# Optimization experiments

Measured on AMD Instinct MI355X. Metric: run time of the kernel, lower is better.

The kernel has to match this reference:

```python
import jax, jax.numpy as jnp
import numpy as np

N_OBJ = 256   # number of RoIs/objects
C = 151       # num_obj_classes (Visual Genome)
H = 512       # hidden_dim == output_dim
T = 3         # time_step


def setup_inputs() -> dict:
    key = jax.random.key(0)
    ks = jax.random.split(key, 12)
    s = jnp.float32(0.02)

    def lin(k, out_dim, in_dim):
        k1, k2 = jax.random.split(k)
        w = jax.random.normal(k1, (out_dim, in_dim), jnp.float32) * s
        b = jax.random.normal(k2, (out_dim,), jnp.float32) * s
        return w, b

    inp = {}
    inp['input_ggnn'] = jax.random.normal(ks[0], (N_OBJ, H), jnp.float32)
    inp['matrix'] = jax.random.uniform(ks[1], (C, C), jnp.float32)
    for i, name in enumerate(['eq3_w', 'eq3_u', 'eq4_w', 'eq4_u', 'eq5_w', 'eq5_u']):
        in_dim = 2 * H if name.endswith('_w') else H
        w, b = lin(ks[2 + i], H, in_dim)
        inp['w_' + name] = w
        inp['b_' + name] = b
    w, b = lin(ks[8], H, 2 * H)
    inp['w_out'], inp['b_out'] = w, b
    w, b = lin(ks[9], C, C * H)
    inp['w_cls'], inp['b_cls'] = w, b
    return inp


def _ggnn_obj(input_ggnn, matrix,
              w_eq3_w, b_eq3_w, w_eq3_u, b_eq3_u,
              w_eq4_w, b_eq4_w, w_eq4_u, b_eq4_u,
              w_eq5_w, b_eq5_w, w_eq5_u, b_eq5_u,
              w_out, b_out, w_cls, b_cls):
    n = input_ggnn.shape[0]
    # hidden[i, c] = input_ggnn[i] for every class slot c  -> [N, C, H]
    hidden0 = jnp.broadcast_to(input_ggnn[:, None, :], (n, C, H))

    def step(hidden, _):
        hidden_sum = hidden.sum(axis=0)                # [C, H]
        x = hidden_sum[None, :, :] - hidden            # [N, C, H]
        # matrix.T @ x_i  and  matrix @ x_i, vectorized over N
        av1 = jnp.einsum('cd,nch->ndh', matrix, x)     # M^T propagation
        av2 = jnp.einsum('dc,nch->ndh', matrix, x)     # M propagation
        av = jnp.concatenate([av1, av2], axis=-1).reshape(n * C, 2 * H)
        h = hidden.reshape(n * C, H)
        zv = jax.nn.sigmoid(av @ w_eq3_w.T + b_eq3_w + h @ w_eq3_u.T + b_eq3_u)
        rv = jax.nn.sigmoid(av @ w_eq4_w.T + b_eq4_w + h @ w_eq4_u.T + b_eq4_u)
        hv = jnp.tanh(av @ w_eq5_w.T + b_eq5_w + (rv * h) @ w_eq5_u.T + b_eq5_u)
        h = (1.0 - zv) * h + zv * hv
        return h.reshape(n, C, H), None

    hidden, _ = jax.lax.scan(step, hidden0, None, length=T)

    inp_rep = hidden0.reshape(n * C, H)                # input repeated per class slot
    out = jnp.concatenate([hidden.reshape(n * C, H), inp_rep], axis=1)  # [N*C, 2H]
    out = jax.nn.relu(out @ w_out.T + b_out)           # [N*C, H]
    obj_dists = out.reshape(n, C * H) @ w_cls.T + b_cls  # [N, C]
    return obj_dists


def reference(input_ggnn, matrix,
              w_eq3_w, b_eq3_w, w_eq3_u, b_eq3_u,
              w_eq4_w, b_eq4_w, w_eq4_u, b_eq4_u,
              w_eq5_w, b_eq5_w, w_eq5_u, b_eq5_u,
              w_out, b_out, w_cls, b_cls):
    return _ggnn_obj(input_ggnn, matrix,
                     w_eq3_w, b_eq3_w, w_eq3_u, b_eq3_u,
                     w_eq4_w, b_eq4_w, w_eq4_u, b_eq4_u,
                     w_eq5_w, b_eq5_w, w_eq5_u, b_eq5_u,
                     w_out, b_out, w_cls, b_cls)
```

## Files before the change

kernel.cpp:

```cpp
#include <hip/hip_runtime.h>


#define C_     151
#define H_     512
#define NOBJ   256
#define NR     38656
#define NCH    64
#define CH     9664
#define CHP    9728
#define KPAD   160
#define KLDS   168
#define KA     2560
#define KV     3584
#define KB     2560

typedef _Float16 half8 __attribute__((ext_vector_type(8)));
typedef _Float16 half4 __attribute__((ext_vector_type(4)));
typedef float    f32x4 __attribute__((ext_vector_type(4)));

__device__ __forceinline__ float sigm(float x) { return 1.f / (1.f + expf(-x)); }

__device__ __forceinline__ void gload16(const void* g, void* l) {
    __builtin_amdgcn_global_load_lds(
        (const __attribute__((address_space(1))) void*)g,
        (__attribute__((address_space(3))) void*)l, 16, 0, 0);
}

__device__ __forceinline__ int kqswz(int s) {
    return 8 * (((s & 3) + 8 - ((s >> 2) & 3) - ((s >> 4) & 3)) & 3);
}
__device__ __forceinline__ int fraswz(int lane) {
    const int lb = lane & 15;
    return lb * 32 + 8 * (((lane >> 4) + lb + (lb >> 2)) & 3);
}

__device__ __forceinline__ half8 loadA8(const _Float16* p) { return *(const half8*)p; }
__device__ __forceinline__ half8 loadA8(const float* p) {
    f32x4 a = *(const f32x4*)p;
    f32x4 b = *(const f32x4*)(p + 4);
    half8 o;
    #pragma unroll
    for (int j = 0; j < 4; ++j) { o[j] = (_Float16)a[j]; o[4 + j] = (_Float16)b[j]; }
    return o;
}

template<int OP, typename AT, bool DUPK>
__global__ __launch_bounds__(256, 2)
void gemm_kernel(const AT* __restrict__ A, int lda,
                 const _Float16* __restrict__ B, int ldb,
                 void* __restrict__ Out, int ldo,
                 const float* __restrict__ bias,
                 const float* __restrict__ bias2,
                 int kchunk, int chunkStride)
{
    constexpr bool A16 = (sizeof(AT) == 2);
    __shared__ _Float16 sA[128 * 32];
    __shared__ _Float16 sB[128 * 32];
    const int tid  = threadIdx.x;
    const int lane = tid & 63;
    const int w    = tid >> 6;
    const int m0   = blockIdx.x * 128;
    const int n0   = blockIdx.y * 128;
    const int kbase = blockIdx.z * kchunk;

    const int s0 = tid, s1 = tid + 256;
    const AT* Ap0 = A + (size_t)(m0 + (s0 >> 2)) * lda + kqswz(s0);
    const AT* Ap1 = A + (size_t)(m0 + (s1 >> 2)) * lda + kqswz(s1);
    const _Float16* Bp0 = B + (size_t)(n0 + (s0 >> 2)) * ldb + kbase + kqswz(s0);
    const _Float16* Bp1 = B + (size_t)(n0 + (s1 >> 2)) * ldb + kbase + kqswz(s1);
    const int la0 = 8 * s0;
    const int la1 = 8 * s1;
    _Float16* lA0 = &sA[w * 512];
    _Float16* lA1 = &sA[2048 + w * 512];
    _Float16* lB0 = &sB[w * 512];
    _Float16* lB1 = &sB[2048 + w * 512];

    f32x4 acc[4][4];
    #pragma unroll
    for (int i = 0; i < 4; ++i)
        #pragma unroll
        for (int j = 0; j < 4; ++j)
            #pragma unroll
            for (int r = 0; r < 4; ++r) acc[i][j][r] = 0.f;

    const int mrow = (w >> 1) * 64;
    const int ncol = (w & 1) * 64;
    const int fra  = fraswz(lane);

    for (int k0 = 0; k0 < kchunk; k0 += 32) {
        int kA;
        if (DUPK) kA = (k0 < 2048) ? k0 : ((k0 < 3072) ? k0 - 2048 : k0 - 1024);
        else      kA = kbase + k0;
        if constexpr (A16) {
            __syncthreads();
            gload16(Ap0 + kA, lA0);
            gload16(Ap1 + kA, lA1);
            gload16(Bp0 + k0, lB0);
            gload16(Bp1 + k0, lB1);
            __syncthreads();
        } else {
            half8 va0 = loadA8(Ap0 + kA);
            half8 va1 = loadA8(Ap1 + kA);
            half8 vb0 = *(const half8*)(Bp0 + k0);
            half8 vb1 = *(const half8*)(Bp1 + k0);
            __syncthreads();
            *(half8*)&sA[la0] = va0;
            *(half8*)&sA[la1] = va1;
            *(half8*)&sB[la0] = vb0;
            *(half8*)&sB[la1] = vb1;
            __syncthreads();
        }
        half8 af[4], bf[4];
        #pragma unroll
        for (int i = 0; i < 4; ++i)
            af[i] = *(const half8*)&sA[(mrow + i * 16) * 32 + fra];
        #pragma unroll
        for (int i = 0; i < 4; ++i)
            bf[i] = *(const half8*)&sB[(ncol + i * 16) * 32 + fra];
        #pragma unroll
        for (int mi = 0; mi < 4; ++mi)
            #pragma unroll
            for (int ni = 0; ni < 4; ++ni)
                acc[mi][ni] = __builtin_amdgcn_mfma_f32_16x16x32_f16(af[mi], bf[ni], acc[mi][ni], 0, 0, 0);
    }

    const size_t zoff = (size_t)blockIdx.z * (size_t)chunkStride;
    #pragma unroll
    for (int mi = 0; mi < 4; ++mi) {
        #pragma unroll
        for (int ni = 0; ni < 4; ++ni) {
            #pragma unroll
            for (int r = 0; r < 4; ++r) {
                const int row = m0 + mrow + mi * 16 + (lane >> 4) * 4 + r;
                const int col = n0 + ncol + ni * 16 + (lane & 15);
                float v = acc[mi][ni][r];
                const size_t o = zoff + (size_t)row * ldo + col;
                if (OP == 0) {
                    ((float*)Out)[o] = v;
                } else if (OP == 1) {
                    ((_Float16*)Out)[o] = (_Float16)v;
                } else {
                    const unsigned n = (unsigned)row / 151u;
                    v += bias[col] + bias2[n * 512u + col];
                    v = v > 0.f ? v : 0.f;
                    ((_Float16*)Out)[o] = (_Float16)v;
                }
            }
        }
    }
}

__global__ __launch_bounds__(512, 2)
void gemm256(const _Float16* __restrict__ A, const _Float16* __restrict__ B,
             _Float16* __restrict__ Out)
{
    constexpr int LDA = KA;
    constexpr int LDB = KB;
    constexpr int LDO = 1536;
    constexpr int NT  = KV / 64;
    __shared__ _Float16 lds[2][32768];

    const int tid  = threadIdx.x;
    const int lane = tid & 63;
    const int w    = tid >> 6;

    const int lin  = blockIdx.y * gridDim.x + blockIdx.x;
    const int xcd  = lin & 7;
    const int sub  = lin >> 3;
    const int wgid = (xcd < 4 ? xcd * 29 : 4 * 29 + (xcd - 4) * 28) + sub;
    const int m0   = (wgid / 6) * 256;
    const int n0   = (wgid % 6) * 256;

    const int tr  = tid >> 3;
    const int swz = ((tid & 7) ^ (tr & 7)) << 3;
    const _Float16* Ap = A + (size_t)(m0 + tr) * LDA + swz;
    const _Float16* Bp = B + (size_t)(n0 + tr) * LDB + swz;
    const int ldsbase = w << 9;

    auto stage = [&](int buf, int kAb, int kBb) {
        _Float16* L = &lds[buf][0];
        #pragma unroll
        for (int h = 0; h < 2; ++h) {
            #pragma unroll
            for (int r = 0; r < 2; ++r) {
                const int ro = h * 128 + r * 64;
                gload16(Ap + (size_t)ro * LDA + kAb, L + h * 8192 + r * 4096 + ldsbase);
                gload16(Bp + (size_t)ro * LDB + kBb, L + 16384 + h * 8192 + r * 4096 + ldsbase);
            }
        }
    };

    const int lb = lane & 15;
    const int lq = lane >> 4;
    auto frag = [&](const _Float16* base, int row0, int ks) -> half8 {
        const int row = row0 + lb;
        const int kg  = ks * 4 + lq;
        return *(const half8*)&base[row * 64 + ((kg ^ (row & 7)) << 3)];
    };

    const int wm = (w >> 2) * 128;
    const int wn = (w & 3) * 64;

    f32x4 acc[8][4];
    #pragma unroll
    for (int i = 0; i < 8; ++i)
        #pragma unroll
        for (int j = 0; j < 4; ++j)
            #pragma unroll
            for (int r = 0; r < 4; ++r) acc[i][j][r] = 0.f;

    half8 aL[4][2], aH[4][2], bA[2][2], bB[2][2];

#define SYNC_LG() do {                                                          \
    asm volatile("s_waitcnt lgkmcnt(0)" ::: "memory");                          \
    __builtin_amdgcn_s_barrier();                                               \
    __builtin_amdgcn_sched_barrier(0);                                          \
} while (0)
#define SYNC_LGVM() do {                                                        \
    asm volatile("s_waitcnt lgkmcnt(0)" ::: "memory");                          \
    asm volatile("s_waitcnt vmcnt(0)" ::: "memory");                            \
    __builtin_amdgcn_s_barrier();                                               \
    __builtin_amdgcn_sched_barrier(0);                                          \
} while (0)
#define PHASE_MFMA(AF, BF, MO, NO) do {                                         \
    __builtin_amdgcn_s_setprio(1);                                              \
    _Pragma("unroll")                                                           \
    for (int i = 0; i < 4; ++i) {                                               \
        _Pragma("unroll")                                                       \
        for (int j = 0; j < 2; ++j) {                                           \
            _Pragma("unroll")                                                   \
            for (int ks = 0; ks < 2; ++ks)                                      \
                acc[(MO) + i][(NO) + j] =                                       \
                    __builtin_amdgcn_mfma_f32_16x16x32_f16(                     \
                        AF[i][ks], BF[j][ks], acc[(MO) + i][(NO) + j], 0, 0, 0);\
        }                                                                       \
    }                                                                           \
    __builtin_amdgcn_s_setprio(0);                                              \
} while (0)

    stage(0, 0, 0);
    asm volatile("s_waitcnt vmcnt(0)" ::: "memory");
    __builtin_amdgcn_s_barrier();
    __builtin_amdgcn_sched_barrier(0);
    #pragma unroll
    for (int i = 0; i < 4; ++i) {
        aL[i][0] = frag(&lds[0][0], wm + i * 16, 0);
        aL[i][1] = frag(&lds[0][0], wm + i * 16, 1);
    }
    #pragma unroll
    for (int j = 0; j < 2; ++j) {
        bA[j][0] = frag(&lds[0][16384], wn + j * 16, 0);
        bA[j][1] = frag(&lds[0][16384], wn + j * 16, 1);
    }

    for (int t = 0; t < NT; ++t) {
        const _Float16* sA  = &lds[t & 1][0];
        const _Float16* sB  = &lds[t & 1][16384];
        const _Float16* sAn = &lds[(t + 1) & 1][0];
        const _Float16* sBn = &lds[(t + 1) & 1][16384];

        SYNC_LG();
        if (t + 1 < NT) {
            const int kk  = (t + 1) * 64;
            const int kAb = (kk < 2048) ? kk : ((kk < 3072) ? kk - 2048 : kk - 1024);
            const int kBb = (kk < 1024) ? kk : kk - 1024;
            stage((t + 1) & 1, kAb, kBb);
        }
        #pragma unroll
        for (int j = 0; j < 2; ++j) {
            bB[j][0] = frag(sB, wn + 32 + j * 16, 0);
            bB[j][1] = frag(sB, wn + 32 + j * 16, 1);
        }
        PHASE_MFMA(aL, bA, 0, 0);

        SYNC_LG();
        #pragma unroll
        for (int i = 0; i < 4; ++i) {
            aH[i][0] = frag(sA, wm + 64 + i * 16, 0);
            aH[i][1] = frag(sA, wm + 64 + i * 16, 1);
        }
        PHASE_MFMA(aL, bB, 0, 2);

        SYNC_LGVM();
        #pragma unroll
        for (int i = 0; i < 4; ++i) {
            aL[i][0] = frag(sAn, wm + i * 16, 0);
            aL[i][1] = frag(sAn, wm + i * 16, 1);
        }
        PHASE_MFMA(aH, bA, 4, 0);

        SYNC_LG();
        #pragma unroll
        for (int j = 0; j < 2; ++j) {
            bA[j][0] = frag(sBn, wn + j * 16, 0);
            bA[j][1] = frag(sBn, wn + j * 16, 1);
        }
        PHASE_MFMA(aH, bB, 4, 2);
    }
#undef SYNC_LG
#undef SYNC_LGVM
#undef PHASE_MFMA

    #pragma unroll
    for (int mi = 0; mi < 8; ++mi) {
        #pragma unroll
        for (int ni = 0; ni < 4; ++ni) {
            #pragma unroll
            for (int r = 0; r < 4; ++r) {
                const int row = m0 + wm + mi * 16 + (lane >> 4) * 4 + r;
                const int col = n0 + wn + ni * 16 + (lane & 15);
                Out[(size_t)row * LDO + col] = (_Float16)acc[mi][ni][r];
            }
        }
    }
}

__global__ __launch_bounds__(256, 2)
void mix_kernel(const float* __restrict__ hid, const float* __restrict__ S,
                const _Float16* __restrict__ MTh, const _Float16* __restrict__ MTl,
                const _Float16* __restrict__ Mrh, const _Float16* __restrict__ Mrl,
                _Float16* __restrict__ AVH, int cbase)
{
    __shared__ _Float16 sxh[64 * KLDS];
    __shared__ _Float16 sxl[64 * KLDS];
    const int n  = blockIdx.x;
    const int h0 = blockIdx.y * 64;
    const int tid = threadIdx.x;

    #pragma unroll
    for (int i = 0; i < 5; ++i) {
        const int s  = tid + 256 * i;
        const int c  = s >> 3;
        const int hg = s & 7;
        half8 oh, ol;
        if (c < C_) {
            const float* hp = &hid[(size_t)(cbase + n * C_ + c) * H_ + h0 + hg * 8];
            const float* sp = &S[c * H_ + h0 + hg * 8];
            half8 hh;
            #pragma unroll
            for (int j = 0; j < 8; ++j) {
                const float hv = hp[j];
                const float x = sp[j] - hv;
                const _Float16 hi = (_Float16)x;
                oh[j] = hi;
                ol[j] = (_Float16)(x - (float)hi);
                hh[j] = (_Float16)hv;
            }
            *(half8*)&AVH[(size_t)(n * C_ + c) * KA + 2048 + h0 + hg * 8] = hh;
        } else {
            #pragma unroll
            for (int j = 0; j < 8; ++j) { oh[j] = (_Float16)0.f; ol[j] = (_Float16)0.f; }
        }
        #pragma unroll
        for (int j = 0; j < 8; ++j) {
            sxh[(hg * 8 + j) * KLDS + c] = oh[j];
            sxl[(hg * 8 + j) * KLDS + c] = ol[j];
        }
    }
    __syncthreads();

    const int lane = tid & 63;
    const int w    = tid >> 6;
    const _Float16* Mhi = (w >> 1) ? Mrh : MTh;
    const _Float16* Mlo = (w >> 1) ? Mrl : MTl;
    const int hb = (w & 1) * 32;

    f32x4 acc[10][2];
    #pragma unroll
    for (int i = 0; i < 10; ++i)
        #pragma unroll
        for (int j = 0; j < 2; ++j)
            #pragma unroll
            for (int r = 0; r < 4; ++r) acc[i][j][r] = 0.f;

    #pragma unroll
    for (int pass = 0; pass < 3; ++pass) {
        const _Float16* Ma = (pass == 2) ? Mlo : Mhi;
        const _Float16* X  = (pass == 1) ? sxl : sxh;
        #pragma unroll
        for (int kk = 0; kk < 5; ++kk) {
            const int k0 = kk * 32;
            half8 bf[2];
            #pragma unroll
            for (int ht = 0; ht < 2; ++ht)
                bf[ht] = *(const half8*)&X[(hb + ht * 16 + (lane & 15)) * KLDS + k0 + 8 * (lane >> 4)];
            #pragma unroll
            for (int dt = 0; dt < 10; ++dt) {
                half8 af = *(const half8*)&Ma[(dt * 16 + (lane & 15)) * KPAD + k0 + 8 * (lane >> 4)];
                acc[dt][0] = __builtin_amdgcn_mfma_f32_16x16x32_f16(af, bf[0], acc[dt][0], 0, 0, 0);
                acc[dt][1] = __builtin_amdgcn_mfma_f32_16x16x32_f16(af, bf[1], acc[dt][1], 0, 0, 0);
            }
        }
    }

    const int mixoff = (w >> 1) * 512;
    #pragma unroll
    for (int dt = 0; dt < 10; ++dt) {
        #pragma unroll
        for (int ht = 0; ht < 2; ++ht) {
            #pragma unroll
            for (int r = 0; r < 4; ++r) {
                const int d = dt * 16 + (lane >> 4) * 4 + r;
                if (d < C_) {
                    const int h = h0 + hb + ht * 16 + (lane & 15);
                    const float v = acc[dt][ht][r];
                    const _Float16 hi = (_Float16)v;
                    const _Float16 lo = (_Float16)(v - (float)hi);
                    _Float16* rowp = AVH + (size_t)(n * C_ + d) * KA + mixoff + h;
                    rowp[0]    = hi;
                    rowp[1024] = lo;
                }
            }
        }
    }
}


__global__ void k_sreduce(const float* __restrict__ hid, float* __restrict__ Stmp)
{
    const int c  = blockIdx.x;
    const int g  = blockIdx.y;
    const int hw = threadIdx.x;
    const float* p = hid + (size_t)c * H_ + hw * 8;
    float s[8];
    #pragma unroll
    for (int j = 0; j < 8; ++j) s[j] = 0.f;
    const size_t stride = (size_t)C_ * H_;
    for (int n = g * 32; n < g * 32 + 32; ++n) {
        f32x4 a = *(const f32x4*)(p + (size_t)n * stride);
        f32x4 b = *(const f32x4*)(p + (size_t)n * stride + 4);
        #pragma unroll
        for (int j = 0; j < 4; ++j) { s[j] += a[j]; s[4 + j] += b[j]; }
    }
    float* o = Stmp + (size_t)g * (C_ * H_) + c * H_ + hw * 8;
    *(f32x4*)o       = f32x4{s[0], s[1], s[2], s[3]};
    *(f32x4*)(o + 4) = f32x4{s[4], s[5], s[6], s[7]};
}

__global__ void k_sfold(const float* __restrict__ Stmp, float* __restrict__ S)
{
    const int idx = blockIdx.x * 256 + threadIdx.x;
    float s = 0.f;
    #pragma unroll
    for (int g = 0; g < 8; ++g) s += Stmp[(size_t)g * (C_ * H_) + idx];
    S[idx] = s;
}

__global__ void k_ew1(_Float16* __restrict__ pre, const float* __restrict__ hid,
                      const float* __restrict__ bz, const float* __restrict__ br, int cbase)
{
    const int idx = blockIdx.x * 256 + threadIdx.x;
    const unsigned r = idx >> 7;
    const int o4 = (idx & 127) << 2;
    const size_t base = (size_t)r * 1536;
    half4 zp = *(const half4*)&pre[base + o4];
    half4 rp = *(const half4*)&pre[base + 512 + o4];
    f32x4 hd = *(const f32x4*)&hid[(size_t)(cbase + r) * H_ + o4];
    f32x4 bz4 = *(const f32x4*)&bz[o4];
    f32x4 br4 = *(const f32x4*)&br[o4];
    half4 zs, rh;
    #pragma unroll
    for (int j = 0; j < 4; ++j) {
        float z = sigm((float)zp[j] + bz4[j]);
        float rr = sigm((float)rp[j] + br4[j]);
        zs[j] = (_Float16)z;
        rh[j] = (_Float16)(rr * hd[j]);
    }
    *(half4*)&pre[base + o4] = zs;
    *(half4*)&pre[base + 512 + o4] = rh;
}

__global__ void k_ew2(const _Float16* __restrict__ pre, const _Float16* __restrict__ p5a,
                      const _Float16* __restrict__ p5b,
                      float* __restrict__ hid, const float* __restrict__ b5, int cbase)
{
    const int idx = blockIdx.x * 256 + threadIdx.x;
    const unsigned r = idx >> 7;
    const int o4 = (idx & 127) << 2;
    const size_t base = (size_t)r * 1536;
    half4 w5 = *(const half4*)&pre[base + 1024 + o4];
    half4 pa = *(const half4*)&p5a[(size_t)r * H_ + o4];
    half4 pb = *(const half4*)&p5b[(size_t)r * H_ + o4];
    half4 zz = *(const half4*)&pre[base + o4];
    f32x4 hd = *(const f32x4*)&hid[(size_t)(cbase + r) * H_ + o4];
    f32x4 b54 = *(const f32x4*)&b5[o4];
    #pragma unroll
    for (int j = 0; j < 4; ++j) {
        float t = tanhf((float)w5[j] + (float)pa[j] + (float)pb[j] + b54[j]);
        float z = (float)zz[j];
        hd[j] = (1.f - z) * hd[j] + z * t;
    }
    *(f32x4*)&hid[(size_t)(cbase + r) * H_ + o4] = hd;
}


__global__ void prep_wbig(const float* w3w, const float* w3u,
                          const float* w4w, const float* w4u,
                          const float* w5w, const float* w5u,
                          _Float16* __restrict__ Wbig)
{
    const int idx = blockIdx.x * 256 + threadIdx.x;
    const int op = idx / KB;
    const int j = idx - op * KB;
    const int g = op >> 9, o = op & 511;
    const float* ww = (g == 0) ? w3w : (g == 1) ? w4w : w5w;
    const float* wu = (g == 0) ? w3u : (g == 1) ? w4u : w5u;
    _Float16 out;
    if (j < 1024) {
        out = (_Float16)ww[o * 1024 + j];
    } else if (j < 2048) {
        const float v = ww[o * 1024 + (j - 1024)];
        const _Float16 hi = (_Float16)v;
        out = (_Float16)(v - (float)hi);
    } else {
        out = (g < 2) ? (_Float16)wu[o * 512 + (j - 2048)] : (_Float16)0.f;
    }
    Wbig[idx] = out;
}

__global__ void prep_m(const float* __restrict__ matrix,
                       _Float16* __restrict__ MTh, _Float16* __restrict__ MTl,
                       _Float16* __restrict__ Mrh, _Float16* __restrict__ Mrl)
{
    const int idx = blockIdx.x * 256 + threadIdx.x;
    const int d = idx / KPAD, c = idx - d * KPAD;
    float vT = 0.f, vR = 0.f;
    if (d < C_ && c < C_) { vT = matrix[c * C_ + d]; vR = matrix[d * C_ + c]; }
    const _Float16 th = (_Float16)vT;
    const _Float16 rh = (_Float16)vR;
    MTh[idx] = th; MTl[idx] = (_Float16)(vT - (float)th);
    Mrh[idx] = rh; Mrl[idx] = (_Float16)(vR - (float)rh);
}

__global__ void prep_wout(const float* __restrict__ wout,
                          _Float16* __restrict__ WL, _Float16* __restrict__ WR)
{
    const int idx = blockIdx.x * 256 + threadIdx.x;
    const int o = idx >> 9, j = idx & 511;
    WL[idx] = (_Float16)wout[o * 1024 + j];
    WR[idx] = (_Float16)wout[o * 1024 + 512 + j];
}

__global__ void prep_wcls(const float* __restrict__ wcls, _Float16* __restrict__ w16)
{
    const int k = blockIdx.x * 256 + threadIdx.x;
    const int d = blockIdx.y;
    w16[(size_t)d * (C_ * H_) + k] = (_Float16)wcls[(size_t)d * (C_ * H_) + k];
}

__global__ void k_cast(const float* __restrict__ src, _Float16* __restrict__ dst, int n)
{
    const int i = blockIdx.x * 256 + threadIdx.x;
    if (i < n) dst[i] = (_Float16)src[i];
}

__global__ void prep_bias(const float* b3w, const float* b3u, const float* b4w,
                          const float* b4u, const float* b5w, const float* b5u,
                          float* bz, float* br, float* b5)
{
    const int i = threadIdx.x;
    bz[i] = b3w[i] + b3u[i];
    br[i] = b4w[i] + b4u[i];
    b5[i] = b5w[i] + b5u[i];
}

__global__ void prep_hid(const float* __restrict__ input, float* __restrict__ hid)
{
    const int idx = blockIdx.x * 256 + threadIdx.x;
    const unsigned row = idx >> 7;
    const int h4 = (idx & 127) << 2;
    const unsigned n = row / 151u;
    f32x4 v = *(const f32x4*)&input[(size_t)n * H_ + h4];
    *(f32x4*)&hid[(size_t)row * H_ + h4] = v;
}

__global__ void k_reduce(const float* __restrict__ partial, const float* __restrict__ bcls,
                         float* __restrict__ out)
{
    const int idx = blockIdx.x * 256 + threadIdx.x;
    const unsigned n = (unsigned)idx / 151u;
    const unsigned d = (unsigned)idx - n * 151u;
    float s = 0.f;
    for (int z = 0; z < C_; ++z)
        s += partial[(size_t)z * (NOBJ * 256) + n * 256 + d];
    out[idx] = s + bcls[d];
}


extern "C" void kernel_launch(void* const* d_in, const int* in_sizes, int n_in,
                              void* d_out, int out_size, void* d_ws, size_t ws_size,
                              hipStream_t stream)
{
    const float* input  = (const float*)d_in[0];
    const float* matrix = (const float*)d_in[1];
    const float* w3w = (const float*)d_in[2];
    const float* b3w = (const float*)d_in[3];
    const float* w3u = (const float*)d_in[4];
    const float* b3u = (const float*)d_in[5];
    const float* w4w = (const float*)d_in[6];
    const float* b4w = (const float*)d_in[7];
    const float* w4u = (const float*)d_in[8];
    const float* b4u = (const float*)d_in[9];
    const float* w5w = (const float*)d_in[10];
    const float* b5w = (const float*)d_in[11];
    const float* w5u = (const float*)d_in[12];
    const float* b5u = (const float*)d_in[13];
    const float* wout = (const float*)d_in[14];
    const float* bout = (const float*)d_in[15];
    const float* wcls = (const float*)d_in[16];
    const float* bcls = (const float*)d_in[17];
    float* obj = (float*)d_out;

    char* ws = (char*)d_ws;
    size_t off = 0;
    auto take = [&](size_t bytes) -> char* {
        off = (off + 255) & ~(size_t)255;
        char* p = ws + off;
        off += bytes;
        return p;
    };

    _Float16* Wbig  = (_Float16*)take((size_t)1536 * KB * 2);
    _Float16* MTh   = (_Float16*)take((size_t)KPAD * KPAD * 2);
    _Float16* MTl   = (_Float16*)take((size_t)KPAD * KPAD * 2);
    _Float16* Mrh   = (_Float16*)take((size_t)KPAD * KPAD * 2);
    _Float16* Mrl   = (_Float16*)take((size_t)KPAD * KPAD * 2);
    _Float16* W5u16 = (_Float16*)take((size_t)512 * 512 * 2);
    _Float16* WL16  = (_Float16*)take((size_t)512 * 512 * 2);
    _Float16* WR16  = (_Float16*)take((size_t)512 * 512 * 2);
    _Float16* in16  = (_Float16*)take((size_t)256 * 512 * 2);
    float*    bz    = (float*)take(512 * 4);
    float*    br    = (float*)take(512 * 4);
    float*    b5    = (float*)take(512 * 4);
    float*    Stmp  = (float*)take((size_t)8 * C_ * H_ * 4);
    float*    S32   = (float*)take((size_t)C_ * H_ * 4);
    float*    base  = (float*)take((size_t)256 * 512 * 4);
    float*    hid32 = (float*)take((size_t)NR * H_ * 4);
    _Float16* AVH   = (_Float16*)take((size_t)CHP * KA * 2);
    _Float16* prec  = (_Float16*)take((size_t)CHP * 1536 * 2);
    _Float16* p5u = AVH;
    _Float16* OUT16 = AVH;
    _Float16* Wcls16 = (_Float16*)hid32;
    float* partial = (float*)((char*)hid32 + (size_t)NOBJ * C_ * H_ * 2);

    (void)in_sizes; (void)n_in; (void)out_size; (void)ws_size;

    prep_wbig<<<dim3((1536 * KB) / 256), 256, 0, stream>>>(w3w, w3u, w4w, w4u, w5w, w5u, Wbig);
    prep_m<<<dim3((KPAD * KPAD) / 256), 256, 0, stream>>>(matrix, MTh, MTl, Mrh, Mrl);
    k_cast<<<dim3((512 * 512) / 256), 256, 0, stream>>>(w5u, W5u16, 512 * 512);
    prep_wout<<<dim3((512 * 512) / 256), 256, 0, stream>>>(wout, WL16, WR16);
    k_cast<<<dim3((256 * 512) / 256), 256, 0, stream>>>(input, in16, 256 * 512);
    prep_bias<<<dim3(1), 512, 0, stream>>>(b3w, b3u, b4w, b4u, b5w, b5u, bz, br, b5);
    prep_hid<<<dim3((NR * 128) / 256), 256, 0, stream>>>(input, hid32);
    gemm_kernel<0, _Float16, false><<<dim3(2, 4, 1), 256, 0, stream>>>(
        in16, 512, WR16, 512, base, 512, nullptr, nullptr, 512, 0);

    for (int t = 0; t < 3; ++t) {
        k_sreduce<<<dim3(C_, 8), 64, 0, stream>>>(hid32, Stmp);
        k_sfold<<<dim3((C_ * H_) / 256), 256, 0, stream>>>(Stmp, S32);
        for (int cc = 0; cc < 4; ++cc) {
            const int cbase = cc * CH;
            mix_kernel<<<dim3(NCH, 8), 256, 0, stream>>>(
                hid32, S32, MTh, MTl, Mrh, Mrl, AVH, cbase);
            gemm256<<<dim3(CHP / 256, 1536 / 256, 1), 512, 0, stream>>>(
                AVH, Wbig, prec);
            k_ew1<<<dim3((CH * 128) / 256), 256, 0, stream>>>(prec, hid32, bz, br, cbase);
            gemm_kernel<1, _Float16, false><<<dim3(CHP / 128, 4, 2), 256, 0, stream>>>(
                prec + 512, 1536, W5u16, 512, p5u, 512, nullptr, nullptr, 256, CHP * 512);
            k_ew2<<<dim3((CH * 128) / 256), 256, 0, stream>>>(
                prec, p5u, p5u + (size_t)CHP * 512, hid32, b5, cbase);
        }
    }

    gemm_kernel<2, float, false><<<dim3(NR / 128, 512 / 128, 1), 256, 0, stream>>>(
        hid32, 512, WL16, 512, OUT16, 512, bout, base, 512, 0);

    prep_wcls<<<dim3((C_ * H_) / 256, C_), 256, 0, stream>>>(wcls, Wcls16);
    gemm_kernel<0, _Float16, false><<<dim3(NOBJ / 128, 256 / 128, C_), 256, 0, stream>>>(
        OUT16, C_ * H_, Wcls16, C_ * H_, partial, 256, nullptr, nullptr, 512, NOBJ * 256);
    k_reduce<<<dim3(NR / 256), 256, 0, stream>>>(partial, bcls, obj);
}
```

Measured before the change: 2.542 ms.

## Restructure GEMM main loop with partial vmcnt waits and fewer barriers

The double-buffered GEMM loop now issues its global-to-LDS loads in an order that puts the rows needed first at the front. It then waits with partial vmcnt counts so the first half of the tile can be consumed while the second half is still arriving. The four barrier phases per iteration become two, and fragments for the current buffer are loaded at the start of each iteration instead of being prefetched from the next buffer. This cuts synchronisation overhead but gives up register prefetch across iterations, so LDS read latency is more exposed. The partial waits rely on the exact load issue order being kept.

Result: faster. 2.416 ms (-5.0%).

```diff
diff --git a/kernel.cpp b/kernel.cpp
--- a/kernel.cpp
+++ b/kernel.cpp
@@ -179,15 +179,14 @@
 
     auto stage = [&](int buf, int kAb, int kBb) {
         _Float16* L = &lds[buf][0];
-        #pragma unroll
-        for (int h = 0; h < 2; ++h) {
-            #pragma unroll
-            for (int r = 0; r < 2; ++r) {
-                const int ro = h * 128 + r * 64;
-                gload16(Ap + (size_t)ro * LDA + kAb, L + h * 8192 + r * 4096 + ldsbase);
-                gload16(Bp + (size_t)ro * LDB + kBb, L + 16384 + h * 8192 + r * 4096 + ldsbase);
-            }
-        }
+        gload16(Ap + kAb,                        L + ldsbase);
+        gload16(Ap + (size_t)128 * LDA + kAb,    L + 128 * 64 + ldsbase);
+        gload16(Bp + kBb,                        L + 16384 + ldsbase);
+        gload16(Bp + (size_t)64  * LDB + kBb,    L + 16384 +  64 * 64 + ldsbase);
+        gload16(Bp + (size_t)128 * LDB + kBb,    L + 16384 + 128 * 64 + ldsbase);
+        gload16(Bp + (size_t)192 * LDB + kBb,    L + 16384 + 192 * 64 + ldsbase);
+        gload16(Ap + (size_t)64  * LDA + kAb,    L +  64 * 64 + ldsbase);
+        gload16(Ap + (size_t)192 * LDA + kAb,    L + 192 * 64 + ldsbase);
     };
 
     const int lb = lane & 15;
@@ -211,17 +210,6 @@
 
     half8 aL[4][2], aH[4][2], bA[2][2], bB[2][2];
 
-#define SYNC_LG() do {                                                          \
-    asm volatile("s_waitcnt lgkmcnt(0)" ::: "memory");                          \
-    __builtin_amdgcn_s_barrier();                                               \
-    __builtin_amdgcn_sched_barrier(0);                                          \
-} while (0)
-#define SYNC_LGVM() do {                                                        \
-    asm volatile("s_waitcnt lgkmcnt(0)" ::: "memory");                          \
-    asm volatile("s_waitcnt vmcnt(0)" ::: "memory");                            \
-    __builtin_amdgcn_s_barrier();                                               \
-    __builtin_amdgcn_sched_barrier(0);                                          \
-} while (0)
 #define PHASE_MFMA(AF, BF, MO, NO) do {                                         \
     __builtin_amdgcn_s_setprio(1);                                              \
     _Pragma("unroll")                                                           \
@@ -239,27 +227,14 @@
 } while (0)
 
     stage(0, 0, 0);
-    asm volatile("s_waitcnt vmcnt(0)" ::: "memory");
-    __builtin_amdgcn_s_barrier();
-    __builtin_amdgcn_sched_barrier(0);
-    #pragma unroll
-    for (int i = 0; i < 4; ++i) {
-        aL[i][0] = frag(&lds[0][0], wm + i * 16, 0);
-        aL[i][1] = frag(&lds[0][0], wm + i * 16, 1);
-    }
-    #pragma unroll
-    for (int j = 0; j < 2; ++j) {
-        bA[j][0] = frag(&lds[0][16384], wn + j * 16, 0);
-        bA[j][1] = frag(&lds[0][16384], wn + j * 16, 1);
-    }
 
     for (int t = 0; t < NT; ++t) {
-        const _Float16* sA  = &lds[t & 1][0];
-        const _Float16* sB  = &lds[t & 1][16384];
-        const _Float16* sAn = &lds[(t + 1) & 1][0];
-        const _Float16* sBn = &lds[(t + 1) & 1][16384];
-
-        SYNC_LG();
+        const _Float16* sA = &lds[t & 1][0];
+        const _Float16* sB = &lds[t & 1][16384];
+
+        asm volatile("s_waitcnt vmcnt(2)" ::: "memory");
+        __builtin_amdgcn_s_barrier();
+        __builtin_amdgcn_sched_barrier(0);
         if (t + 1 < NT) {
             const int kk  = (t + 1) * 64;
             const int kAb = (kk < 2048) ? kk : ((kk < 3072) ? kk - 2048 : kk - 1024);
@@ -267,38 +242,35 @@
             stage((t + 1) & 1, kAb, kBb);
         }
         #pragma unroll
+        for (int i = 0; i < 4; ++i) {
+            aL[i][0] = frag(sA, wm + i * 16, 0);
+            aL[i][1] = frag(sA, wm + i * 16, 1);
+        }
+        #pragma unroll
+        for (int j = 0; j < 2; ++j) {
+            bA[j][0] = frag(sB, wn + j * 16, 0);
+            bA[j][1] = frag(sB, wn + j * 16, 1);
+        }
+        #pragma unroll
         for (int j = 0; j < 2; ++j) {
             bB[j][0] = frag(sB, wn + 32 + j * 16, 0);
             bB[j][1] = frag(sB, wn + 32 + j * 16, 1);
         }
         PHASE_MFMA(aL, bA, 0, 0);
-
-        SYNC_LG();
+        PHASE_MFMA(aL, bB, 0, 2);
+
+        if (t + 1 < NT) asm volatile("s_waitcnt vmcnt(8)" ::: "memory");
+        else            asm volatile("s_waitcnt vmcnt(0)" ::: "memory");
+        __builtin_amdgcn_s_barrier();
+        __builtin_amdgcn_sched_barrier(0);
         #pragma unroll
         for (int i = 0; i < 4; ++i) {
             aH[i][0] = frag(sA, wm + 64 + i * 16, 0);
             aH[i][1] = frag(sA, wm + 64 + i * 16, 1);
         }
-        PHASE_MFMA(aL, bB, 0, 2);
-
-        SYNC_LGVM();
-        #pragma unroll
-        for (int i = 0; i < 4; ++i) {
-            aL[i][0] = frag(sAn, wm + i * 16, 0);
-            aL[i][1] = frag(sAn, wm + i * 16, 1);
-        }
         PHASE_MFMA(aH, bA, 4, 0);
-
-        SYNC_LG();
-        #pragma unroll
-        for (int j = 0; j < 2; ++j) {
-            bA[j][0] = frag(sBn, wn + j * 16, 0);
-            bA[j][1] = frag(sBn, wn + j * 16, 1);
-        }
         PHASE_MFMA(aH, bB, 4, 2);
     }
-#undef SYNC_LG
-#undef SYNC_LGVM
 #undef PHASE_MFMA
 
     #pragma unroll
```
